# Performance work log

Hardware: AMD Instinct MI355X
Metric: run time of the kernel (lower is better)

Reference implementation:

```python
import jax, jax.numpy as jnp
import numpy as np

T_DEC = 60  # decoder steps, hard-coded in the original forward

def _conv1d(x, w, b):
    # x: [B, C_in, L], w: [C_out, C_in, K] -> [B, C_out, L-K+1] (valid conv)
    y = jax.lax.conv_general_dilated(x, w, window_strides=(1,), padding='VALID',
                                     dimension_numbers=('NCH', 'OIH', 'NCH'))
    return y + b[None, :, None]

def _lstm_cell(x, h, c, wih, whh, bih, bhh):
    # PyTorch LSTM cell, gate order i, f, g, o
    g = x @ wih.T + h @ whh.T + (bih + bhh)
    i, f, gg, o = jnp.split(g, 4, axis=-1)
    c = jax.nn.sigmoid(f) * c + jax.nn.sigmoid(i) * jnp.tanh(gg)
    h = jax.nn.sigmoid(o) * jnp.tanh(c)
    return h, c

def _lstm_seq(xs, wih, whh, bih, bhh, reverse=False):
    # xs: [B, T, D] -> [B, T, H], zero initial state (PyTorch default)
    B, H = xs.shape[0], whh.shape[1]
    xs_t = jnp.swapaxes(xs, 0, 1)
    if reverse:
        xs_t = xs_t[::-1]
    def step(carry, x):
        h, c = carry
        h, c = _lstm_cell(x, h, c, wih, whh, bih, bhh)
        return (h, c), h
    init = (jnp.zeros((B, H), xs.dtype), jnp.zeros((B, H), xs.dtype))
    _, hs = jax.lax.scan(step, init, xs_t)
    if reverse:
        hs = hs[::-1]
    return jnp.swapaxes(hs, 0, 1)

def setup_inputs():
    key = jax.random.key(0)
    B, L, D_in, H, D_out = 64, 4096, 64, 256, 128
    C1, C2, C3 = 8, 16, 32
    ks = jax.random.split(key, 32)
    it = iter(ks)
    def p(shape, scale=0.1):
        return jax.random.normal(next(it), shape, jnp.float32) * scale
    inp = {}
    inp['x'] = jax.random.normal(next(it), (B, L, D_in), jnp.float32)
    inp['conv_w1'] = p((C1, D_in, 4)); inp['conv_b1'] = p((C1,))
    inp['conv_w2'] = p((C2, C1, 8));  inp['conv_b2'] = p((C2,))
    inp['conv_w3'] = p((C3, C2, 16)); inp['conv_b3'] = p((C3,))
    inp['attn_w'] = p((H, C3)); inp['attn_b'] = p((H,))
    inp['dec1_wih'] = p((2, 4 * H, C3)); inp['dec1_whh'] = p((2, 4 * H, H))
    inp['dec1_bih'] = p((2, 4 * H));     inp['dec1_bhh'] = p((2, 4 * H))
    inp['dec2_wih0'] = p((2, 4 * H, 2 * H)); inp['dec2_whh0'] = p((2, 4 * H, H))
    inp['dec2_bih0'] = p((2, 4 * H));        inp['dec2_bhh0'] = p((2, 4 * H))
    inp['dec2_wih1'] = p((2, 4 * H, 2 * H)); inp['dec2_whh1'] = p((2, 4 * H, H))
    inp['dec2_bih1'] = p((2, 4 * H));        inp['dec2_bhh1'] = p((2, 4 * H))
    inp['out_w'] = p((D_out, 2 * H)); inp['out_b'] = p((D_out,))
    return inp

def reference(x, conv_w1, conv_b1, conv_w2, conv_b2, conv_w3, conv_b3,
              attn_w, attn_b, dec1_wih, dec1_whh, dec1_bih, dec1_bhh,
              dec2_wih0, dec2_whh0, dec2_bih0, dec2_bhh0,
              dec2_wih1, dec2_whh1, dec2_bih1, dec2_bhh1, out_w, out_b):
    # Eval mode: all dropouts are identity.
    h = jnp.swapaxes(x, 1, 2)  # [B, D_in, L]
    h = jax.nn.relu(_conv1d(h, conv_w1, conv_b1))
    h = jax.nn.relu(_conv1d(h, conv_w2, conv_b2))
    h = jax.nn.relu(_conv1d(h, conv_w3, conv_b3))
    enc = jnp.swapaxes(h, 1, 2)  # [B, Lp, 32], Lp = L - 25
    keys_t = jnp.einsum('blc,hc->bhl', enc, attn_w) + attn_b[None, :, None]  # [B, H, Lp]
    B, H = x.shape[0], attn_w.shape[0]

    def dec1(wih, whh, bih, bhh):
        def step(carry, _):
            hh, cc = carry
            align = jnp.einsum('bh,bhl->bl', hh, keys_t)   # attention scores over Lp
            a = jax.nn.softmax(align, axis=-1)
            ctx = jnp.einsum('bl,blc->bc', a, enc)         # context [B, 32]
            hh, cc = _lstm_cell(ctx, hh, cc, wih, whh, bih, bhh)
            return (hh, cc), hh
        init = (jnp.zeros((B, H), x.dtype), jnp.zeros((B, H), x.dtype))
        _, hs = jax.lax.scan(step, init, None, length=T_DEC)
        return jnp.swapaxes(hs, 0, 1)  # [B, 60, H]

    fwd = dec1(dec1_wih[0], dec1_whh[0], dec1_bih[0], dec1_bhh[0])
    # the bkwd branch writes step i into slot 60-i-1, i.e. time-reversed outputs
    bkwd = dec1(dec1_wih[1], dec1_whh[1], dec1_bih[1], dec1_bhh[1])[:, ::-1]
    d2in = jnp.concatenate([fwd, bkwd], axis=-1)  # [B, 60, 2H]
    l0 = jnp.concatenate([
        _lstm_seq(d2in, dec2_wih0[0], dec2_whh0[0], dec2_bih0[0], dec2_bhh0[0]),
        _lstm_seq(d2in, dec2_wih0[1], dec2_whh0[1], dec2_bih0[1], dec2_bhh0[1], reverse=True)], axis=-1)
    l1 = jnp.concatenate([
        _lstm_seq(l0, dec2_wih1[0], dec2_whh1[0], dec2_bih1[0], dec2_bhh1[0]),
        _lstm_seq(l0, dec2_wih1[1], dec2_whh1[1], dec2_bih1[1], dec2_bhh1[1], reverse=True)], axis=-1)
    return l1 @ out_w.T + out_b  # [B, 60, D_out]
```

## Files before the change

kernel.cpp:

```cpp
#include <hip/hip_runtime.h>

#define B_    64
#define L1C   4093
#define L2C   4086
#define L3C   4071
#define TDEC  60

static __device__ __forceinline__ float sigf(float x){ return 1.f/(1.f + __expf(-x)); }

typedef _Float16 h2_t __attribute__((ext_vector_type(2)));
union U2H { unsigned u; h2_t h; };

static __device__ __forceinline__ unsigned pkh2(float a, float b){
  U2H r; r.h[0] = (_Float16)a; r.h[1] = (_Float16)b; return r.u;
}
static __device__ __forceinline__ float dot2f(unsigned w, unsigned h, float acc){
  U2H a; a.u = w; U2H b; b.u = h;
#if __has_builtin(__builtin_amdgcn_fdot2)
  return __builtin_amdgcn_fdot2(a.h, b.h, acc, false);
#else
  acc = fmaf((float)a.h[0], (float)b.h[0], acc);
  acc = fmaf((float)a.h[1], (float)b.h[1], acc);
  return acc;
#endif
}

#define DOT8(g, wv, hv) \
  g = dot2f(wv.x, hv.x, g); g = dot2f(wv.y, hv.y, g); \
  g = dot2f(wv.z, hv.z, g); g = dot2f(wv.w, hv.w, g);

template<int CIN,int COUT,int KW>
__global__ __launch_bounds__(256) void k_conv(
    const float* __restrict__ in, const float* __restrict__ w,
    const float* __restrict__ bias, float* __restrict__ outp,
    int Lin_, int Lout_)
{
  int g = blockIdx.x*256 + threadIdx.x;
  int bi = g / Lout_;
  int l  = g - bi*Lout_;
  if (bi >= B_) return;
  float acc[COUT];
#pragma unroll
  for (int o=0;o<COUT;o++) acc[o] = bias[o];
  const float* ip = in + ((size_t)bi*Lin_ + l)*CIN;
  for (int k=0;k<KW;k++){
#pragma unroll
    for (int i4=0;i4<CIN/4;i4++){
      float4 xv = *(const float4*)(ip + k*CIN + i4*4);
#pragma unroll
      for (int c=0;c<4;c++){
        float xs = (&xv.x)[c];
        int i = i4*4+c;
#pragma unroll
        for (int o=0;o<COUT;o++)
          acc[o] = fmaf(xs, w[(o*CIN + i)*KW + k], acc[o]);
      }
    }
  }
  float* op = outp + ((size_t)bi*Lout_ + l)*COUT;
#pragma unroll
  for (int o=0;o<COUT;o++) op[o] = fmaxf(acc[o],0.f);
}

__global__ __launch_bounds__(256) void k_conv3q(
    const float* __restrict__ in, const float* __restrict__ w,
    const float* __restrict__ bias, uint4* __restrict__ encq,
    float* __restrict__ encs, int Lin_, int Lout_)
{
  int g = blockIdx.x*256 + threadIdx.x;
  int bi = g / Lout_;
  int l  = g - bi*Lout_;
  if (bi >= B_) return;
  float acc[32];
#pragma unroll
  for (int o=0;o<32;o++) acc[o] = bias[o];
  const float* ip = in + ((size_t)bi*Lin_ + l)*16;
  for (int k=0;k<16;k++){
#pragma unroll
    for (int i4=0;i4<4;i4++){
      float4 xv = *(const float4*)(ip + k*16 + i4*4);
#pragma unroll
      for (int c=0;c<4;c++){
        float xs = (&xv.x)[c];
        int i = i4*4+c;
#pragma unroll
        for (int o=0;o<32;o++)
          acc[o] = fmaf(xs, w[(o*16 + i)*16 + k], acc[o]);
      }
    }
  }
  float mx = 0.f;
#pragma unroll
  for (int o=0;o<32;o++){ acc[o] = fmaxf(acc[o],0.f); mx = fmaxf(mx, acc[o]); }
  float scale = mx * (1.f/255.f);
  float inv = (mx > 0.f) ? (255.f/mx) : 0.f;
  unsigned qs[8];
#pragma unroll
  for (int q8=0;q8<8;q8++){
    unsigned q0 = (unsigned)(acc[q8*4+0]*inv + 0.5f);
    unsigned q1 = (unsigned)(acc[q8*4+1]*inv + 0.5f);
    unsigned q2 = (unsigned)(acc[q8*4+2]*inv + 0.5f);
    unsigned q3 = (unsigned)(acc[q8*4+3]*inv + 0.5f);
    qs[q8] = q0 | (q1<<8) | (q2<<16) | (q3<<24);
  }
  uint4* op = encq + ((size_t)bi*Lout_ + l)*2;
  op[0] = make_uint4(qs[0],qs[1],qs[2],qs[3]);
  op[1] = make_uint4(qs[4],qs[5],qs[6],qs[7]);
  encs[(size_t)bi*Lout_ + l] = scale;
}

__global__ __launch_bounds__(256) void k_packwh(
    const float* __restrict__ w, uint4* __restrict__ wT, int K)
{
  int gid = blockIdx.x*256 + threadIdx.x;
  int per = (K/8)*1024;
  int d = gid / per, rem = gid - d*per;
  int j8 = rem >> 10, row = rem & 1023;
  const float* src = w + ((size_t)d*1024 + row)*K + j8*8;
  float4 a = *(const float4*)src;
  float4 b = *(const float4*)(src+4);
  uint4 o;
  o.x = pkh2(a.x, a.y);
  o.y = pkh2(a.z, a.w);
  o.z = pkh2(b.x, b.y);
  o.w = pkh2(b.z, b.w);
  wT[gid] = o;
}

#define CVT8(r, qv) \
  r[0]=(float)( qv.x      & 255u); r[1]=(float)((qv.x>>8 ) & 255u); \
  r[2]=(float)((qv.x>>16) & 255u); r[3]=(float)((qv.x>>24)       ); \
  r[4]=(float)( qv.y      & 255u); r[5]=(float)((qv.y>>8 ) & 255u); \
  r[6]=(float)((qv.y>>16) & 255u); r[7]=(float)((qv.y>>24)       );

__global__ __launch_bounds__(1024) void k_dec1g(
    const uint4* __restrict__ encq,
    const float* __restrict__ encs,
    const float* __restrict__ attn_w,
    const uint4* __restrict__ wihT,
    const uint4* __restrict__ whhT,
    const float* __restrict__ bih, const float* __restrict__ bhh,
    float* __restrict__ d2in)
{
  int b = blockIdx.x, d = blockIdx.y, tid = threadIdx.x;
  int c = tid & 3, rb = tid >> 2;

  __shared__ __align__(16) uint2 encQ2[16384];
  __shared__ float sls[4096];
  __shared__ __align__(16) float hls[256];
  __shared__ __align__(16) unsigned h2pk[128];
  __shared__ __align__(16) unsigned ctxh[16];
  __shared__ float vl[32];
  __shared__ float maxenc[32];
  __shared__ float Msh;
  __shared__ float red[1024];
  __shared__ float scr[512];
  __shared__ float gls[1024];

  {
    const uint4* src = encq + (size_t)b*L3C*2;
    uint4* dst = (uint4*)encQ2;
    for (int i = tid; i < 8192; i += 1024)
      dst[i] = (i < L3C*2) ? src[i] : make_uint4(0,0,0,0);
    const float* ss = encs + (size_t)b*L3C;
    for (int i = tid; i < 4096; i += 1024)
      sls[i] = (i < L3C) ? ss[i] : 0.f;
  }
  if (tid < 256) hls[tid] = 0.f;
  if (tid < 128) h2pk[tid] = 0u;
  float creg = 0.f;
  float bsum = bih[(size_t)d*1024 + tid] + bhh[(size_t)d*1024 + tid];
  const uint4* whp = whhT + (size_t)d*32768;
  __syncthreads();

  {
    float mc[8];
#pragma unroll
    for (int j=0;j<8;j++) mc[j] = 0.f;
#pragma unroll
    for (int k=0;k<16;k++){
      int l = rb + 256*k;
      uint2 qv = encQ2[l*4 + c];
      float sl = sls[l];
      float r[8]; CVT8(r, qv)
#pragma unroll
      for (int j=0;j<8;j++) mc[j] = fmaxf(mc[j], r[j]*sl);
    }
#pragma unroll
    for (int off=4; off<=32; off<<=1){
#pragma unroll
      for (int j=0;j<8;j++) mc[j] = fmaxf(mc[j], __shfl_xor(mc[j], off));
    }
    int wid = tid >> 6;
    if ((tid&63) < 4){
#pragma unroll
      for (int j=0;j<8;j++) scr[wid*32 + c*8 + j] = mc[j];
    }
    __syncthreads();
    if (tid < 32){
      float mm = 0.f;
#pragma unroll
      for (int w=0;w<16;w++) mm = fmaxf(mm, scr[w*32 + tid]);
      maxenc[tid] = mm;
    }
    __syncthreads();
  }

  for (int t=0; t<TDEC; t++){
    {
      int cc = tid & 31, part = tid >> 5;
      const float* wp = attn_w + (size_t)(part*8)*32 + cc;
      float s = 0.f;
#pragma unroll
      for (int k=0;k<8;k++) s = fmaf(hls[part*8+k], wp[k*32], s);
      red[tid] = s;
    }
    __syncthreads();
    if (tid < 32){
      float v = 0.f;
#pragma unroll
      for (int q=0;q<32;q++) v += red[q*32 + tid];
      vl[tid] = v;
      float mt = maxenc[tid] * fmaxf(v, 0.f);
#pragma unroll
      for (int off=1; off<32; off<<=1) mt += __shfl_xor(mt, off);
      if (tid==0) Msh = mt;
    }
    __syncthreads();

    float vreg[8];
#pragma unroll
    for (int j=0;j<8;j++) vreg[j] = vl[c*8 + j];
    float M = Msh;
    float ssum = 0.f;
    float acc[8];
#pragma unroll
    for (int j=0;j<8;j++) acc[j] = 0.f;
#pragma unroll
    for (int k=0;k<16;k++){
      int l = rb + 256*k;
      uint2 qv = encQ2[l*4 + c];
      float sl = sls[l];
      float r[8]; CVT8(r, qv)
      float s = 0.f;
#pragma unroll
      for (int j=0;j<8;j++) s = fmaf(r[j], vreg[j], s);
      s += __shfl_xor(s, 1);
      s += __shfl_xor(s, 2);
      s *= sl;
      if (k==15 && l >= L3C) s = -3.0e38f;
      float e = __expf(s - M);
      ssum += e;
      float em = e * sl;
#pragma unroll
      for (int j=0;j<8;j++) acc[j] = fmaf(em, r[j], acc[j]);
    }
#pragma unroll
    for (int off=4; off<=32; off<<=1){
      ssum += __shfl_xor(ssum, off);
#pragma unroll
      for (int j=0;j<8;j++) acc[j] += __shfl_xor(acc[j], off);
    }
    int wid = tid >> 6;
    if ((tid&63) < 4){
#pragma unroll
      for (int j=0;j<8;j++) scr[wid*32 + c*8 + j] = acc[j];
    }
    if ((tid&63)==0) red[wid] = ssum;
    __syncthreads();
    if (tid < 32){
      float S = 0.f, s2 = 0.f;
#pragma unroll
      for (int w=0;w<16;w++){ S += red[w]; s2 += scr[w*32 + tid]; }
      float cv = s2 / S;
      float co = __shfl_xor(cv, 1);
      if (!(tid&1)) ctxh[tid>>1] = pkh2(cv, co);
    }
    __syncthreads();

    float g = bsum;
#pragma unroll
    for (int c8=0;c8<4;c8++){
      uint4 wv = wihT[(size_t)d*4096 + c8*1024 + tid];
      uint4 hv = *(const uint4*)&ctxh[c8*4];
      DOT8(g, wv, hv)
    }
#pragma unroll 8
    for (int j8=0;j8<32;j8++){
      uint4 wv = whp[j8*1024 + tid];
      uint4 hv = *(const uint4*)&h2pk[j8*4];
      DOT8(g, wv, hv)
    }
    gls[tid] = g;
    __syncthreads();
    if (tid < 256){
      float ii = sigf(gls[tid]);
      float ff = sigf(gls[256+tid]);
      float gg = tanhf(gls[512+tid]);
      float oo = sigf(gls[768+tid]);
      creg = fmaf(ff, creg, ii*gg);
      float hn = oo * tanhf(creg);
      hls[tid] = hn;
      float ho = __shfl_xor(hn, 1);
      if (!(tid&1)) h2pk[tid>>1] = pkh2(hn, ho);
      int tout = d ? (59 - t) : t;
      d2in[((size_t)b*60 + tout)*512 + d*256 + tid] = hn;
    }
    __syncthreads();
  }
}

__global__ __launch_bounds__(256) void k_gemm(
    const float* __restrict__ A, const float* __restrict__ W,
    float* __restrict__ C, const float* __restrict__ b1, const float* __restrict__ b2,
    int K, int ldc, size_t sW, size_t sC, int sB)
{
  int m0 = blockIdx.x * 128, n0 = blockIdx.y * 128, z = blockIdx.z;
  const float* Wz = W + (size_t)z*sW;
  float* Cz = C + (size_t)z*sC;
  const float* b1z = b1 + (size_t)z*sB;
  const float* b2z = b2 ? (b2 + (size_t)z*sB) : nullptr;
  __shared__ __align__(16) float As[16][132];
  __shared__ __align__(16) float Bs[16][132];
  int tid = threadIdx.x;
  int tx = tid & 15, ty = tid >> 4;
  int r = tid >> 2, c4 = tid & 3;
  float acc[8][8] = {};
  for (int k0=0; k0<K; k0+=16){
#pragma unroll
    for (int h=0; h<2; h++){
      int rr = r + h*64;
      float4 av = *(const float4*)(A  + (size_t)(m0+rr)*K + k0 + c4*4);
      float4 bv = *(const float4*)(Wz + (size_t)(n0+rr)*K + k0 + c4*4);
      As[c4*4+0][rr]=av.x; As[c4*4+1][rr]=av.y; As[c4*4+2][rr]=av.z; As[c4*4+3][rr]=av.w;
      Bs[c4*4+0][rr]=bv.x; Bs[c4*4+1][rr]=bv.y; Bs[c4*4+2][rr]=bv.z; Bs[c4*4+3][rr]=bv.w;
    }
    __syncthreads();
#pragma unroll
    for (int kk=0; kk<16; kk++){
      float a[8], bb[8];
      *(float4*)&a[0]  = *(const float4*)&As[kk][ty*8];
      *(float4*)&a[4]  = *(const float4*)&As[kk][ty*8+4];
      *(float4*)&bb[0] = *(const float4*)&Bs[kk][tx*8];
      *(float4*)&bb[4] = *(const float4*)&Bs[kk][tx*8+4];
#pragma unroll
      for (int i=0;i<8;i++)
#pragma unroll
        for (int j=0;j<8;j++)
          acc[i][j] = fmaf(a[i], bb[j], acc[i][j]);
    }
    __syncthreads();
  }
  float bb1[8];
#pragma unroll
  for (int j=0;j<8;j++){
    int n = n0 + tx*8 + j;
    bb1[j] = b1z[n] + (b2z ? b2z[n] : 0.f);
  }
#pragma unroll
  for (int i=0;i<8;i++){
    int m = m0 + ty*8 + i;
    float o[8];
#pragma unroll
    for (int j=0;j<8;j++) o[j] = acc[i][j] + bb1[j];
    *(float4*)(Cz + (size_t)m*ldc + n0 + tx*8)     = *(const float4*)&o[0];
    *(float4*)(Cz + (size_t)m*ldc + n0 + tx*8 + 4) = *(const float4*)&o[4];
  }
}

__global__ __launch_bounds__(1024) void k_rec2(
    const float* __restrict__ xg,
    const uint4* __restrict__ wT,
    float* __restrict__ out)
{
  int b = blockIdx.x, d = blockIdx.y, tid = threadIdx.x;
  __shared__ __align__(16) unsigned h2pk[128];
  __shared__ float gls[1024];
  float c = 0.f;
  if (tid < 128) h2pk[tid] = 0u;
  __syncthreads();
  const uint4* wp = wT + (size_t)d*32*1024;
  const float* xp = xg + (((size_t)d*64 + b)*60)*1024;
  for (int step=0; step<TDEC; step++){
    int t = d ? (TDEC-1-step) : step;
    float g = xp[(size_t)t*1024 + tid];
#pragma unroll 8
    for (int j8=0;j8<32;j8++){
      uint4 wv = wp[j8*1024 + tid];
      uint4 hv = *(const uint4*)&h2pk[j8*4];
      DOT8(g, wv, hv)
    }
    gls[tid] = g;
    __syncthreads();
    if (tid < 256){
      float ii = sigf(gls[tid]);
      float ff = sigf(gls[256+tid]);
      float gg = tanhf(gls[512+tid]);
      float oo = sigf(gls[768+tid]);
      c = fmaf(ff, c, ii*gg);
      float hn = oo * tanhf(c);
      float ho = __shfl_xor(hn, 1);
      if (!(tid&1)) h2pk[tid>>1] = pkh2(hn, ho);
      out[((size_t)b*60 + t)*512 + d*256 + tid] = hn;
    }
    __syncthreads();
  }
}

extern "C" void kernel_launch(void* const* d_in, const int* in_sizes, int n_in,
                              void* d_out, int out_size, void* d_ws, size_t ws_size,
                              hipStream_t stream) {
  const float* x      = (const float*)d_in[0];
  const float* cw1    = (const float*)d_in[1];
  const float* cb1    = (const float*)d_in[2];
  const float* cw2    = (const float*)d_in[3];
  const float* cb2    = (const float*)d_in[4];
  const float* cw3    = (const float*)d_in[5];
  const float* cb3    = (const float*)d_in[6];
  const float* attn_w = (const float*)d_in[7];
  const float* d1_wih = (const float*)d_in[9];
  const float* d1_whh = (const float*)d_in[10];
  const float* d1_bih = (const float*)d_in[11];
  const float* d1_bhh = (const float*)d_in[12];
  const float* w2_ih0 = (const float*)d_in[13];
  const float* w2_hh0 = (const float*)d_in[14];
  const float* b2_ih0 = (const float*)d_in[15];
  const float* b2_hh0 = (const float*)d_in[16];
  const float* w2_ih1 = (const float*)d_in[17];
  const float* w2_hh1 = (const float*)d_in[18];
  const float* b2_ih1 = (const float*)d_in[19];
  const float* b2_hh1 = (const float*)d_in[20];
  const float* out_w  = (const float*)d_in[21];
  const float* out_b  = (const float*)d_in[22];

  char* ws = (char*)d_ws;
  size_t off = 0;
  uint4* encq = (uint4*)(ws + off);
  float* encs = (float*)(ws + off + 8338432);
  off += 16675840;
  size_t off_h1 = off;
  float* h1buf = (float*)(ws + off); off += 8382464;
  float* h2buf = (float*)(ws + off); off += 16736256;
  float* d2in  = (float*)(ws + off_h1);
  float* l0    = (float*)(ws + off_h1 + 7864320);
  float* l1    = (float*)(ws + off_h1 + 15728640);
  uint4* wT    = (uint4*)(ws + off_h1 + 23592960);
  float* xg    = (float*)(ws + off); off += 31457280;
  uint4* d1whhT = (uint4*)xg;
  uint4* d1wihT = (uint4*)((char*)xg + 1048576);
  (void)ws_size; (void)in_sizes; (void)n_in; (void)out_size;

  k_packwh<<<256,256,0,stream>>>(d1_whh, d1whhT, 256);
  k_packwh<<<32, 256,0,stream>>>(d1_wih, d1wihT, 32);

  int g1 = (B_*L1C + 255)/256;
  k_conv<64,8,4><<<g1,256,0,stream>>>(x, cw1, cb1, h1buf, 4096, L1C);
  int g2 = (B_*L2C + 255)/256;
  k_conv<8,16,8><<<g2,256,0,stream>>>(h1buf, cw2, cb2, h2buf, L1C, L2C);
  int g3 = (B_*L3C + 255)/256;
  k_conv3q<<<g3,256,0,stream>>>(h2buf, cw3, cb3, encq, encs, L2C, L3C);

  k_dec1g<<<dim3(64,2),1024,0,stream>>>(encq, encs, attn_w, d1wihT, d1whhT,
                                        d1_bih, d1_bhh, d2in);

  k_packwh<<<256,256,0,stream>>>(w2_hh0, wT, 256);
  k_gemm<<<dim3(30,8,2),256,0,stream>>>(d2in, w2_ih0, xg, b2_ih0, b2_hh0,
                                        512, 1024, (size_t)1024*512, (size_t)3840*1024, 1024);
  k_rec2<<<dim3(64,2),1024,0,stream>>>(xg, wT, l0);
  k_packwh<<<256,256,0,stream>>>(w2_hh1, wT, 256);
  k_gemm<<<dim3(30,8,2),256,0,stream>>>(l0, w2_ih1, xg, b2_ih1, b2_hh1,
                                        512, 1024, (size_t)1024*512, (size_t)3840*1024, 1024);
  k_rec2<<<dim3(64,2),1024,0,stream>>>(xg, wT, l1);
  k_gemm<<<dim3(30,1,1),256,0,stream>>>(l1, out_w, (float*)d_out, out_b, nullptr,
                                        512, 128, 0, 0, 0);
}
```

Measured before the change: 2.004 ms.

## Overlap recurrent h-projection with attention loop, use DPP reductions, cache half of Whh in registers

In the decoder-1 step kernel, the recurrent Whh·h dot products are interleaved into the attention softmax/context loop so their weight loads overlap with the attention math. Cross-lane shuffles for the small reductions are replaced with DPP row operations. In k_rec2, the first half of the packed Whh slice is preloaded into 16 uint4 registers per thread and reused across all 60 timesteps, cutting per-step global or L2 weight traffic. The register cache raises register pressure at 1024 threads per block, which risks spills, and the masking condition now runs on every iteration.

```diff
diff --git a/kernel.cpp b/kernel.cpp
--- a/kernel.cpp
+++ b/kernel.cpp
@@ -28,6 +28,12 @@
 #define DOT8(g, wv, hv) \
   g = dot2f(wv.x, hv.x, g); g = dot2f(wv.y, hv.y, g); \
   g = dot2f(wv.z, hv.z, g); g = dot2f(wv.w, hv.w, g);
+
+template<int CTRL>
+static __device__ __forceinline__ float dppadd(float x){
+  int y = __builtin_amdgcn_update_dpp(0, __float_as_int(x), CTRL, 0xf, 0xf, true);
+  return x + __int_as_float(y);
+}
 
 template<int CIN,int COUT,int KW>
 __global__ __launch_bounds__(256) void k_conv(
@@ -236,8 +242,11 @@
     float acc[8];
 #pragma unroll
     for (int j=0;j<8;j++) acc[j] = 0.f;
-#pragma unroll
+    float g = bsum;
+#pragma unroll 4
     for (int k=0;k<16;k++){
+      uint4 wv0 = whp[(2*k  )*1024 + tid];
+      uint4 wv1 = whp[(2*k+1)*1024 + tid];
       int l = rb + 256*k;
       uint2 qv = encQ2[l*4 + c];
       float sl = sls[l];
@@ -245,21 +254,26 @@
       float s = 0.f;
 #pragma unroll
       for (int j=0;j<8;j++) s = fmaf(r[j], vreg[j], s);
-      s += __shfl_xor(s, 1);
-      s += __shfl_xor(s, 2);
+      s = dppadd<0xB1>(s);
+      s = dppadd<0x4E>(s);
       s *= sl;
-      if (k==15 && l >= L3C) s = -3.0e38f;
+      if (l >= L3C) s = -3.0e38f;
       float e = __expf(s - M);
       ssum += e;
       float em = e * sl;
 #pragma unroll
       for (int j=0;j<8;j++) acc[j] = fmaf(em, r[j], acc[j]);
-    }
-#pragma unroll
-    for (int off=4; off<=32; off<<=1){
-      ssum += __shfl_xor(ssum, off);
-#pragma unroll
-      for (int j=0;j<8;j++) acc[j] += __shfl_xor(acc[j], off);
+      uint4 hv0 = *(const uint4*)&h2pk[(2*k  )*4];
+      uint4 hv1 = *(const uint4*)&h2pk[(2*k+1)*4];
+      DOT8(g, wv0, hv0)
+      DOT8(g, wv1, hv1)
+    }
+    ssum = dppadd<0x124>(ssum); ssum = dppadd<0x128>(ssum);
+    ssum += __shfl_xor(ssum, 16); ssum += __shfl_xor(ssum, 32);
+#pragma unroll
+    for (int j=0;j<8;j++){
+      acc[j] = dppadd<0x124>(acc[j]); acc[j] = dppadd<0x128>(acc[j]);
+      acc[j] += __shfl_xor(acc[j], 16); acc[j] += __shfl_xor(acc[j], 32);
     }
     int wid = tid >> 6;
     if ((tid&63) < 4){
@@ -278,17 +292,10 @@
     }
     __syncthreads();
 
-    float g = bsum;
 #pragma unroll
     for (int c8=0;c8<4;c8++){
       uint4 wv = wihT[(size_t)d*4096 + c8*1024 + tid];
       uint4 hv = *(const uint4*)&ctxh[c8*4];
-      DOT8(g, wv, hv)
-    }
-#pragma unroll 8
-    for (int j8=0;j8<32;j8++){
-      uint4 wv = whp[j8*1024 + tid];
-      uint4 hv = *(const uint4*)&h2pk[j8*4];
       DOT8(g, wv, hv)
     }
     gls[tid] = g;
@@ -378,14 +385,22 @@
   __shared__ float gls[1024];
   float c = 0.f;
   if (tid < 128) h2pk[tid] = 0u;
+  const uint4* wp = wT + (size_t)d*32*1024;
+  uint4 wpre[16];
+#pragma unroll
+  for (int j=0;j<16;j++) wpre[j] = wp[j*1024 + tid];
+  const float* xp = xg + (((size_t)d*64 + b)*60)*1024;
   __syncthreads();
-  const uint4* wp = wT + (size_t)d*32*1024;
-  const float* xp = xg + (((size_t)d*64 + b)*60)*1024;
   for (int step=0; step<TDEC; step++){
     int t = d ? (TDEC-1-step) : step;
     float g = xp[(size_t)t*1024 + tid];
-#pragma unroll 8
-    for (int j8=0;j8<32;j8++){
+#pragma unroll
+    for (int j8=0;j8<16;j8++){
+      uint4 hv = *(const uint4*)&h2pk[j8*4];
+      DOT8(g, wpre[j8], hv)
+    }
+#pragma unroll 4
+    for (int j8=16;j8<32;j8++){
       uint4 wv = wp[j8*1024 + tid];
       uint4 hv = *(const uint4*)&h2pk[j8*4];
       DOT8(g, wv, hv)
```

Measured after the change: 1.606 ms. -19.9%, faster.
